# Kernel tuning notes

Hardware: AMD Instinct MI355X
Metric: run time of the kernel (lower is better)

The kernel has to match this reference:

```python
import jax, jax.numpy as jnp
import numpy as np

N = 100000
C_IN = 256          # in_channels == out_channels * expansion -> identity downsample
C_MID = 64          # out_channels
C_OUT = 256         # out_channels * expansion
K = 27              # 3x3x3 kernel offsets
EPS = 1e-6


def setup_inputs() -> dict:
    key = jax.random.key(0)
    ks = jax.random.split(key, 8)
    feats = jax.random.normal(ks[0], (N, C_IN), dtype=jnp.float32)
    neighbor_idx = jax.random.randint(ks[1], (N, K), 0, N, dtype=jnp.int32)
    # conv weights (torchsparse Conv3d: no bias)
    W1 = jax.random.normal(ks[2], (C_IN, C_MID), dtype=jnp.float32) * (1.0 / np.sqrt(C_IN))
    W2 = jax.random.normal(ks[3], (K, C_MID, C_MID), dtype=jnp.float32) * (1.0 / np.sqrt(K * C_MID))
    W3 = jax.random.normal(ks[4], (C_MID, C_OUT), dtype=jnp.float32) * (1.0 / np.sqrt(C_MID))
    # LayerNorm params
    g1 = jnp.ones((C_MID,), jnp.float32); b1 = jnp.zeros((C_MID,), jnp.float32)
    g2 = jnp.ones((C_MID,), jnp.float32); b2 = jnp.zeros((C_MID,), jnp.float32)
    g3 = jnp.ones((C_OUT,), jnp.float32); b3 = jnp.zeros((C_OUT,), jnp.float32)
    return {"feats": feats, "neighbor_idx": neighbor_idx,
            "W1": W1, "g1": g1, "b1": b1,
            "W2": W2, "g2": g2, "b2": b2,
            "W3": W3, "g3": g3, "b3": b3}


def _layernorm(x, g, b):
    # per-point LayerNorm over channel dim, eps=1e-6
    mu = jnp.mean(x, axis=-1, keepdims=True)
    var = jnp.mean(jnp.square(x - mu), axis=-1, keepdims=True)
    return (x - mu) * jax.lax.rsqrt(var + EPS) * g + b


def reference(feats, neighbor_idx, W1, g1, b1, W2, g2, b2, W3, g3, b3):
    # conv1 (1x1x1): per-point matmul -> LN -> ReLU
    h = jax.nn.relu(_layernorm(feats @ W1, g1, b1))               # [N, C_MID]
    # conv2 (3x3x3 sparse): gather neighbors, contract over (k, c)
    gathered = h[neighbor_idx]                                     # [N, K, C_MID]
    h2 = jnp.einsum('nkc,kcd->nd', gathered, W2)                   # [N, C_MID]
    h2 = jax.nn.relu(_layernorm(h2, g2, b2))
    # conv3 (1x1x1) -> LN
    h3 = _layernorm(h2 @ W3, g3, b3)                               # [N, C_OUT]
    # identity downsample (in_channels == out_channels*expansion, stride=1)
    return jax.nn.relu(h3 + feats)
```

## Files before the change

kernel.cpp:

```cpp
#include <hip/hip_runtime.h>

#define NPTS 100000
typedef unsigned short u16;
typedef __attribute__((ext_vector_type(8))) short short8;
typedef __attribute__((ext_vector_type(4))) float floatx4;

#define HOFF     (1u << 20)
#define H2OFF    (HOFF + 25600000u)
#define WS_NEED  (H2OFF + 25600000u)

__device__ __forceinline__ float bf2f(u16 u) {
    union { unsigned i; float f; } v; v.i = ((unsigned)u) << 16; return v.f;
}
__device__ __forceinline__ u16 f2bf(float f) {
    union { float fv; unsigned i; } v; v.fv = f;
    unsigned x = v.i;
    return (u16)((x + 0x7FFFu + ((x >> 16) & 1u)) >> 16);
}
__device__ __forceinline__ bool probe_bf16(const void* g1) {
    return ((const u16*)g1)[0] == 0x3F80u;
}
template<bool BF> __device__ __forceinline__ float ldf(const void* p, size_t i) {
    if constexpr (BF) return bf2f(((const u16*)p)[i]);
    else return ((const float*)p)[i];
}

template<bool BF> __device__ __forceinline__ void stout(char* ob, int r, int c, float v) {
    if constexpr (BF) ((u16*)(ob + (size_t)r * 512))[c] = f2bf(v);
    else ((float*)(ob + (size_t)r * 1024))[c] = v;
}

template<bool BF> __device__ __forceinline__ void prep_impl(
    const void* W2, const void* W1, const void* W3,
    u16* W2H, u16* W2L, u16* W1TH, u16* W1TL, u16* W3TH, u16* W3TL, int i)
{
    if (i < 27 * 4096) {
        int k = i >> 12, r = i & 4095, d = r >> 6, c = r & 63;
        float w = ldf<BF>(W2, (size_t)k * 4096 + c * 64 + d);
        u16 h = f2bf(w);
        W2H[i] = h;
        W2L[i] = f2bf(w - bf2f(h));
    } else if (i < 27 * 4096 + 16384) {
        int j = i - 27 * 4096;
        int d = j >> 8, k = j & 255;
        float w = ldf<BF>(W1, (size_t)k * 64 + d);
        u16 h = f2bf(w);
        W1TH[j] = h;
        W1TL[j] = f2bf(w - bf2f(h));
    } else if (i < 27 * 4096 + 32768) {
        int j = i - 27 * 4096 - 16384;
        int c = j >> 6, d = j & 63;
        float w = ldf<BF>(W3, (size_t)d * 256 + c);
        u16 h = f2bf(w);
        W3TH[j] = h;
        W3TL[j] = f2bf(w - bf2f(h));
    }
}
__global__ __launch_bounds__(256) void prep_k(const void* W2, const void* W1, const void* W3,
                                              const void* g1,
                                              u16* W2H, u16* W2L, u16* W1TH, u16* W1TL,
                                              u16* W3TH, u16* W3TL) {
    int i = blockIdx.x * 256 + threadIdx.x;
    if (probe_bf16(g1)) prep_impl<true >(W2, W1, W3, W2H, W2L, W1TH, W1TL, W3TH, W3TL, i);
    else                prep_impl<false>(W2, W1, W3, W2H, W2L, W1TH, W1TL, W3TH, W3TL, i);
}

template<bool BF> __device__ __forceinline__ void k1_impl(
    const void* feats, const u16* __restrict__ W1TH, const u16* __restrict__ W1TL,
    const void* g1, const void* b1, char* ob, u16* hb, int dense, u16* BH)
{
    u16* hbase = dense ? hb : (u16*)(ob + (BF ? 256 : 512));
    const int hpitch = dense ? 128 : (BF ? 256 : 512);

    const int tid = threadIdx.x;
    const int blk0 = blockIdx.x * 64;

    for (int j = tid; j < 2048; j += 256) {
        int d = j >> 5, c0 = (j & 31) * 8;
        *(int4*)&BH[d * 264 + c0] = ((const int4*)W1TH)[j];
    }
    __syncthreads();

    const int wave = tid >> 6, lane = tid & 63;
    const int q = lane >> 4, l15 = lane & 15;
    int pr = blk0 + wave * 16 + l15;
    if (pr >= NPTS) pr = NPTS - 1;

    floatx4 acc[4] = {};
    #pragma unroll
    for (int ks = 0; ks < 8; ++ks) {
        const int k0 = ks * 32;
        short8 ahi, alo;
        if constexpr (BF) {
            ahi = *(const short8*)((const u16*)feats + (size_t)pr * 256 + k0 + q * 8);
        } else {
            const float* fp = (const float*)feats + (size_t)pr * 256 + k0 + q * 8;
            float4 f0 = *(const float4*)fp;
            float4 f1 = *(const float4*)(fp + 4);
            float fv[8] = {f0.x, f0.y, f0.z, f0.w, f1.x, f1.y, f1.z, f1.w};
            #pragma unroll
            for (int j = 0; j < 8; ++j) {
                u16 h = f2bf(fv[j]);
                ahi[j] = (short)h;
                alo[j] = (short)f2bf(fv[j] - bf2f(h));
            }
        }
        #pragma unroll
        for (int t = 0; t < 4; ++t) {
            short8 bhi = *(const short8*)&BH[(t * 16 + l15) * 264 + k0 + q * 8];
            acc[t] = __builtin_amdgcn_mfma_f32_16x16x32_bf16(ahi, bhi, acc[t], 0, 0, 0);
            if constexpr (!BF) {
                short8 blo = *(const short8*)(W1TL + (size_t)(t * 16 + l15) * 256 + k0 + q * 8);
                acc[t] = __builtin_amdgcn_mfma_f32_16x16x32_bf16(alo, bhi, acc[t], 0, 0, 0);
                acc[t] = __builtin_amdgcn_mfma_f32_16x16x32_bf16(ahi, blo, acc[t], 0, 0, 0);
                acc[t] = __builtin_amdgcn_mfma_f32_16x16x32_bf16(alo, blo, acc[t], 0, 0, 0);
            }
        }
    }

    float gch[4], bch[4];
    #pragma unroll
    for (int t = 0; t < 4; ++t) { gch[t] = ldf<BF>(g1, t * 16 + l15); bch[t] = ldf<BF>(b1, t * 16 + l15); }

    const int p0 = blk0 + wave * 16;
    #pragma unroll
    for (int r = 0; r < 4; ++r) {
        float x0 = acc[0][r], x1 = acc[1][r], x2 = acc[2][r], x3 = acc[3][r];
        float s1 = x0 + x1 + x2 + x3;
        #pragma unroll
        for (int o = 1; o < 16; o <<= 1) s1 += __shfl_xor(s1, o);
        float mu = s1 * (1.f / 64.f);
        float c0 = x0 - mu, c1 = x1 - mu, c2 = x2 - mu, c3 = x3 - mu;
        float s2 = c0 * c0 + c1 * c1 + c2 * c2 + c3 * c3;
        #pragma unroll
        for (int o = 1; o < 16; o <<= 1) s2 += __shfl_xor(s2, o);
        float rs = rsqrtf(s2 * (1.f / 64.f) + 1e-6f);
        int prow = p0 + q * 4 + r;
        if (prow < NPTS) {
            u16* hp = hbase + (size_t)prow * hpitch;
            float cc[4] = {c0, c1, c2, c3};
            #pragma unroll
            for (int t = 0; t < 4; ++t) {
                float v = cc[t] * rs * gch[t] + bch[t];
                v = v > 0.f ? v : 0.f;
                int d = t * 16 + l15;
                u16 hi = f2bf(v);
                hp[d]      = hi;
                hp[64 + d] = f2bf(v - bf2f(hi));
            }
        }
    }
}
__global__ __launch_bounds__(256) void k1_k(const void* feats, const u16* W1TH, const u16* W1TL,
                                            const void* g1, const void* b1, char* ob,
                                            u16* hb, int dense)
{
    __shared__ __align__(16) u16 BH[64 * 264];
    if (probe_bf16(g1)) k1_impl<true >(feats, W1TH, W1TL, g1, b1, ob, hb, dense, BH);
    else                k1_impl<false>(feats, W1TH, W1TL, g1, b1, ob, hb, dense, BH);
}

__device__ __forceinline__ void k2_epilogue(
    floatx4* acc, const float* gch, const float* bch,
    float* h2base, int h2pitch, int p0, int q, int l15)
{
    #pragma unroll
    for (int r = 0; r < 4; ++r) {
        float x0 = acc[0][r], x1 = acc[1][r], x2 = acc[2][r], x3 = acc[3][r];
        float s1 = x0 + x1 + x2 + x3;
        #pragma unroll
        for (int o = 1; o < 16; o <<= 1) s1 += __shfl_xor(s1, o);
        float mu = s1 * (1.f / 64.f);
        float c0 = x0 - mu, c1 = x1 - mu, c2 = x2 - mu, c3 = x3 - mu;
        float s2 = c0 * c0 + c1 * c1 + c2 * c2 + c3 * c3;
        #pragma unroll
        for (int o = 1; o < 16; o <<= 1) s2 += __shfl_xor(s2, o);
        float rs = rsqrtf(s2 * (1.f / 64.f) + 1e-6f);
        int prow = p0 + q * 4 + r;
        if (prow < NPTS) {
            float* pp = h2base + (size_t)prow * h2pitch;
            float cc[4] = {c0, c1, c2, c3};
            #pragma unroll
            for (int t = 0; t < 4; ++t) {
                float v = cc[t] * rs * gch[t] + bch[t];
                pp[t * 16 + l15] = v > 0.f ? v : 0.f;
            }
        }
    }
}

__global__ __launch_bounds__(256) void k2bf_k(const int* __restrict__ nidx, const u16* __restrict__ W2H,
                                              const void* g2, const void* b2,
                                              const void* g1, char* ob, u16* hb, float* h2b, int dense)
{
    if (!probe_bf16(g1)) return;
    __shared__ __align__(16) u16 Bs[2 * 64 * 72];
    __shared__ int lidx[64 * 27];

    const u16* hbase = dense ? hb : (const u16*)(ob + 256);
    const int hpitch = dense ? 128 : 256;
    float* h2base = dense ? h2b : (float*)ob;
    const int h2pitch = dense ? 64 : 128;

    const int tid = threadIdx.x;
    const int blk0 = blockIdx.x * 64;

    for (int j = tid; j < 64 * 27; j += 256) {
        int p = blk0 + j / 27;
        if (p >= NPTS) p = NPTS - 1;
        lidx[j] = nidx[(size_t)p * 27 + (j % 27)];
    }

    const int wave = tid >> 6, lane = tid & 63;
    const int q = lane >> 4, l15 = lane & 15;
    const int ml = wave * 16 + l15;

    const int sd0 = (tid >> 3) * 72 + (tid & 7) * 8;
    const int sd1 = sd0 + 32 * 72;

    {
        int4 a0 = ((const int4*)W2H)[tid];
        int4 a1 = ((const int4*)W2H)[tid + 256];
        *(int4*)&Bs[sd0] = a0;
        *(int4*)&Bs[sd1] = a1;
    }
    __syncthreads();

    const u16* hp0 = hbase + (size_t)lidx[ml * 27] * hpitch;
    short8 ah0 = *(const short8*)(hp0 + q * 8);
    short8 ah1 = *(const short8*)(hp0 + 32 + q * 8);
    short8 al0 = *(const short8*)(hp0 + 64 + q * 8);
    short8 al1 = *(const short8*)(hp0 + 96 + q * 8);

    floatx4 acc[4] = {};
    int cur = 0;
    #pragma unroll 2
    for (int k = 0; k < 27; ++k) {
        const bool more = (k < 26);
        int4 nh0, nh1;
        if (more) {
            const int4* sH = (const int4*)(W2H + (size_t)(k + 1) * 4096);
            nh0 = sH[tid];
            nh1 = sH[tid + 256];
        }
        short8 ca0 = ah0, ca1 = ah1, cl0 = al0, cl1 = al1;
        if (more) {
            const u16* hn = hbase + (size_t)lidx[ml * 27 + k + 1] * hpitch;
            ah0 = *(const short8*)(hn + q * 8);
            ah1 = *(const short8*)(hn + 32 + q * 8);
            al0 = *(const short8*)(hn + 64 + q * 8);
            al1 = *(const short8*)(hn + 96 + q * 8);
        }
        __builtin_amdgcn_sched_barrier(0);
        const u16* BH = Bs + cur * 4608;
        #pragma unroll
        for (int t = 0; t < 4; ++t) {
            short8 b0 = *(const short8*)&BH[(t * 16 + l15) * 72 + q * 8];
            short8 b1 = *(const short8*)&BH[(t * 16 + l15) * 72 + 32 + q * 8];
            acc[t] = __builtin_amdgcn_mfma_f32_16x16x32_bf16(ca0, b0, acc[t], 0, 0, 0);
            acc[t] = __builtin_amdgcn_mfma_f32_16x16x32_bf16(ca1, b1, acc[t], 0, 0, 0);
            acc[t] = __builtin_amdgcn_mfma_f32_16x16x32_bf16(cl0, b0, acc[t], 0, 0, 0);
            acc[t] = __builtin_amdgcn_mfma_f32_16x16x32_bf16(cl1, b1, acc[t], 0, 0, 0);
        }
        if (more) {
            u16* dH = Bs + (cur ^ 1) * 4608;
            *(int4*)&dH[sd0] = nh0;
            *(int4*)&dH[sd1] = nh1;
        }
        __syncthreads();
        cur ^= 1;
    }

    float gch[4], bch[4];
    #pragma unroll
    for (int t = 0; t < 4; ++t) { gch[t] = ldf<true>(g2, t * 16 + l15); bch[t] = ldf<true>(b2, t * 16 + l15); }
    k2_epilogue(acc, gch, bch, h2base, h2pitch, blk0 + wave * 16, q, l15);
}

__global__ __launch_bounds__(256) void k2f32_k(const int* __restrict__ nidx,
                                               const u16* __restrict__ W2H, const u16* __restrict__ W2L,
                                               const void* g2, const void* b2,
                                               const void* g1, char* ob, u16* hb, float* h2b, int dense)
{
    if (probe_bf16(g1)) return;
    __shared__ __align__(16) u16 Bs[2 * 64 * 72];
    __shared__ int lidx[64 * 27];
    u16* BsH = Bs;
    u16* BsL = Bs + 4608;

    const u16* hbase = dense ? hb : (const u16*)(ob + 512);
    const int hpitch = dense ? 128 : 512;
    float* h2base = dense ? h2b : (float*)(ob + 768);
    const int h2pitch = dense ? 64 : 256;

    const int tid = threadIdx.x;
    const int blk0 = blockIdx.x * 64;

    for (int j = tid; j < 64 * 27; j += 256) {
        int p = blk0 + j / 27;
        if (p >= NPTS) p = NPTS - 1;
        lidx[j] = nidx[(size_t)p * 27 + (j % 27)];
    }
    __syncthreads();

    const int wave = tid >> 6, lane = tid & 63;
    const int q = lane >> 4, l15 = lane & 15;
    const int ml = wave * 16 + l15;

    const u16* hp0 = hbase + (size_t)lidx[ml * 27] * hpitch;
    short8 ah0 = *(const short8*)(hp0 + q * 8);
    short8 ah1 = *(const short8*)(hp0 + 32 + q * 8);
    short8 al0 = *(const short8*)(hp0 + 64 + q * 8);
    short8 al1 = *(const short8*)(hp0 + 96 + q * 8);

    floatx4 acc[4] = {};
    for (int k = 0; k < 27; ++k) {
        __syncthreads();
        for (int j = tid; j < 512; j += 256) {
            int d = j >> 3, c0 = (j & 7) * 8;
            *(int4*)&BsH[d * 72 + c0] = ((const int4*)(W2H + (size_t)k * 4096))[j];
        }
        for (int j = tid; j < 512; j += 256) {
            int d = j >> 3, c0 = (j & 7) * 8;
            *(int4*)&BsL[d * 72 + c0] = ((const int4*)(W2L + (size_t)k * 4096))[j];
        }
        __syncthreads();

        short8 ca0 = ah0, ca1 = ah1, cl0 = al0, cl1 = al1;
        if (k < 26) {
            const u16* hn = hbase + (size_t)lidx[ml * 27 + k + 1] * hpitch;
            ah0 = *(const short8*)(hn + q * 8);
            ah1 = *(const short8*)(hn + 32 + q * 8);
            al0 = *(const short8*)(hn + 64 + q * 8);
            al1 = *(const short8*)(hn + 96 + q * 8);
        }
        #pragma unroll
        for (int t = 0; t < 4; ++t) {
            short8 b0 = *(const short8*)&BsH[(t * 16 + l15) * 72 + q * 8];
            short8 b1 = *(const short8*)&BsH[(t * 16 + l15) * 72 + 32 + q * 8];
            acc[t] = __builtin_amdgcn_mfma_f32_16x16x32_bf16(ca0, b0, acc[t], 0, 0, 0);
            acc[t] = __builtin_amdgcn_mfma_f32_16x16x32_bf16(ca1, b1, acc[t], 0, 0, 0);
            acc[t] = __builtin_amdgcn_mfma_f32_16x16x32_bf16(cl0, b0, acc[t], 0, 0, 0);
            acc[t] = __builtin_amdgcn_mfma_f32_16x16x32_bf16(cl1, b1, acc[t], 0, 0, 0);
            short8 bl0 = *(const short8*)&BsL[(t * 16 + l15) * 72 + q * 8];
            short8 bl1 = *(const short8*)&BsL[(t * 16 + l15) * 72 + 32 + q * 8];
            acc[t] = __builtin_amdgcn_mfma_f32_16x16x32_bf16(ca0, bl0, acc[t], 0, 0, 0);
            acc[t] = __builtin_amdgcn_mfma_f32_16x16x32_bf16(ca1, bl1, acc[t], 0, 0, 0);
        }
    }

    float gch[4], bch[4];
    #pragma unroll
    for (int t = 0; t < 4; ++t) { gch[t] = ldf<false>(g2, t * 16 + l15); bch[t] = ldf<false>(b2, t * 16 + l15); }
    k2_epilogue(acc, gch, bch, h2base, h2pitch, blk0 + wave * 16, q, l15);
}

template<bool BF> __device__ __forceinline__ void k3_impl(
    const void* feats, const u16* __restrict__ W3TH, const u16* __restrict__ W3TL,
    const void* g3, const void* b3, char* ob, float* h2b, int dense, u16* BH)
{
    const float* h2base = dense ? h2b : (const float*)(ob + (BF ? 0 : 768));
    const int h2pitch = dense ? 64 : (BF ? 128 : 256);

    const int tid = threadIdx.x;
    const int blk0 = blockIdx.x * 64;

    for (int j = tid; j < 2048; j += 256) {
        int d = j >> 3, c0 = (j & 7) * 8;
        *(int4*)&BH[d * 72 + c0] = ((const int4*)W3TH)[j];
    }
    __syncthreads();

    const int wave = tid >> 6, lane = tid & 63;
    const int q = lane >> 4, l15 = lane & 15;
    int pr = blk0 + wave * 16 + l15;
    if (pr >= NPTS) pr = NPTS - 1;
    const float* h2p = h2base + (size_t)pr * h2pitch;

    floatx4 acc[16] = {};
    #pragma unroll
    for (int ks = 0; ks < 2; ++ks) {
        const int k0 = ks * 32;
        short8 ahi, alo;
        {
            const float* fp = h2p + k0 + q * 8;
            float4 f0 = *(const float4*)fp;
            float4 f1 = *(const float4*)(fp + 4);
            float fv[8] = {f0.x, f0.y, f0.z, f0.w, f1.x, f1.y, f1.z, f1.w};
            #pragma unroll
            for (int j = 0; j < 8; ++j) {
                u16 h = f2bf(fv[j]);
                ahi[j] = (short)h;
                alo[j] = (short)f2bf(fv[j] - bf2f(h));
            }
        }
        #pragma unroll
        for (int t = 0; t < 16; ++t) {
            short8 bhi = *(const short8*)&BH[(t * 16 + l15) * 72 + k0 + q * 8];
            acc[t] = __builtin_amdgcn_mfma_f32_16x16x32_bf16(ahi, bhi, acc[t], 0, 0, 0);
            acc[t] = __builtin_amdgcn_mfma_f32_16x16x32_bf16(alo, bhi, acc[t], 0, 0, 0);
            if constexpr (!BF) {
                short8 blo = *(const short8*)(W3TL + (size_t)(t * 16 + l15) * 64 + k0 + q * 8);
                acc[t] = __builtin_amdgcn_mfma_f32_16x16x32_bf16(ahi, blo, acc[t], 0, 0, 0);
                acc[t] = __builtin_amdgcn_mfma_f32_16x16x32_bf16(alo, blo, acc[t], 0, 0, 0);
            }
        }
    }

    float gch[16], bch[16];
    #pragma unroll
    for (int t = 0; t < 16; ++t) { gch[t] = ldf<BF>(g3, t * 16 + l15); bch[t] = ldf<BF>(b3, t * 16 + l15); }

    const int p0 = blk0 + wave * 16;
    #pragma unroll
    for (int r = 0; r < 4; ++r) {
        int prow = p0 + q * 4 + r;
        float s1 = 0.f;
        #pragma unroll
        for (int t = 0; t < 16; ++t) s1 += acc[t][r];
        #pragma unroll
        for (int o = 1; o < 16; o <<= 1) s1 += __shfl_xor(s1, o);
        float mu = s1 * (1.f / 256.f);
        float xc[16], s2 = 0.f;
        #pragma unroll
        for (int t = 0; t < 16; ++t) { xc[t] = acc[t][r] - mu; s2 += xc[t] * xc[t]; }
        #pragma unroll
        for (int o = 1; o < 16; o <<= 1) s2 += __shfl_xor(s2, o);
        float rs = rsqrtf(s2 * (1.f / 256.f) + 1e-6f);
        if (prow < NPTS) {
            #pragma unroll
            for (int t = 0; t < 16; ++t) {
                int c = t * 16 + l15;
                float v = xc[t] * rs * gch[t] + bch[t] + ldf<BF>(feats, (size_t)prow * 256 + c);
                stout<BF>(ob, prow, c, v > 0.f ? v : 0.f);
            }
        }
    }
}
__global__ __launch_bounds__(256) void k3_k(const void* feats, const u16* W3TH, const u16* W3TL,
                                            const void* g3, const void* b3,
                                            const void* g1, char* ob, float* h2b, int dense)
{
    __shared__ __align__(16) u16 BH[256 * 72];
    if (probe_bf16(g1)) k3_impl<true >(feats, W3TH, W3TL, g3, b3, ob, h2b, dense, BH);
    else                k3_impl<false>(feats, W3TH, W3TL, g3, b3, ob, h2b, dense, BH);
}

extern "C" void kernel_launch(void* const* d_in, const int* in_sizes, int n_in,
                              void* d_out, int out_size, void* d_ws, size_t ws_size,
                              hipStream_t stream) {
    const void* feats = d_in[0];
    const int*  nidx  = (const int*)d_in[1];
    const void* W1 = d_in[2];
    const void* g1 = d_in[3];
    const void* b1 = d_in[4];
    const void* W2 = d_in[5];
    const void* g2 = d_in[6];
    const void* b2 = d_in[7];
    const void* W3 = d_in[8];
    const void* g3 = d_in[9];
    const void* b3 = d_in[10];
    char* ob = (char*)d_out;

    char* ws = (char*)d_ws;
    u16* W2H  = (u16*)ws;
    u16* W2L  = (u16*)(ws + 221184);
    u16* W1TH = (u16*)(ws + 442368);
    u16* W1TL = (u16*)(ws + 475136);
    u16* W3TH = (u16*)(ws + 507904);
    u16* W3TL = (u16*)(ws + 540672);

    const int dense = (ws_size >= (size_t)WS_NEED) ? 1 : 0;
    u16*   hb  = (u16*)(ws + HOFF);
    float* h2b = (float*)(ws + H2OFF);

    prep_k<<<(27 * 4096 + 32768 + 255) / 256, 256, 0, stream>>>(W2, W1, W3, g1,
                                                                W2H, W2L, W1TH, W1TL, W3TH, W3TL);

    const int nblk = (NPTS + 63) / 64;
    k1_k<<<nblk, 256, 0, stream>>>(feats, W1TH, W1TL, g1, b1, ob, hb, dense);
    k2bf_k<<<nblk, 256, 0, stream>>>(nidx, W2H, g2, b2, g1, ob, hb, h2b, dense);
    k2f32_k<<<nblk, 256, 0, stream>>>(nidx, W2H, W2L, g2, b2, g1, ob, hb, h2b, dense);
    k3_k<<<nblk, 256, 0, stream>>>(feats, W3TH, W3TL, g3, b3, g1, ob, h2b, dense);
}
```

Before: 480.8 us.

## Double-buffer W2 high-half in LDS and read low-half weights from global

The fp32-path sparse conv kernel now prefetches the next kernel offset's high-part weights into registers and writes them into an alternate LDS buffer after the MFMAs. This removes one barrier per iteration and overlaps the weight fetch with compute. The low-part weights are read directly from global/L2 per lane instead of being staged in LDS. This trades LDS traffic and a sync for extra global-load latency inside the MFMA loop.

```diff
diff --git a/kernel.cpp b/kernel.cpp
--- a/kernel.cpp
+++ b/kernel.cpp
@@ -285,8 +285,6 @@
     if (probe_bf16(g1)) return;
     __shared__ __align__(16) u16 Bs[2 * 64 * 72];
     __shared__ int lidx[64 * 27];
-    u16* BsH = Bs;
-    u16* BsL = Bs + 4608;
 
     const u16* hbase = dense ? hb : (const u16*)(ob + 512);
     const int hpitch = dense ? 128 : 512;
@@ -301,11 +299,21 @@
         if (p >= NPTS) p = NPTS - 1;
         lidx[j] = nidx[(size_t)p * 27 + (j % 27)];
     }
-    __syncthreads();
 
     const int wave = tid >> 6, lane = tid & 63;
     const int q = lane >> 4, l15 = lane & 15;
     const int ml = wave * 16 + l15;
+
+    const int sd0 = (tid >> 3) * 72 + (tid & 7) * 8;
+    const int sd1 = sd0 + 32 * 72;
+
+    {
+        int4 a0 = ((const int4*)W2H)[tid];
+        int4 a1 = ((const int4*)W2H)[tid + 256];
+        *(int4*)&Bs[sd0] = a0;
+        *(int4*)&Bs[sd1] = a1;
+    }
+    __syncthreads();
 
     const u16* hp0 = hbase + (size_t)lidx[ml * 27] * hpitch;
     short8 ah0 = *(const short8*)(hp0 + q * 8);
@@ -314,39 +322,47 @@
     short8 al1 = *(const short8*)(hp0 + 96 + q * 8);
 
     floatx4 acc[4] = {};
+    int cur = 0;
+    #pragma unroll 2
     for (int k = 0; k < 27; ++k) {
-        __syncthreads();
-        for (int j = tid; j < 512; j += 256) {
-            int d = j >> 3, c0 = (j & 7) * 8;
-            *(int4*)&BsH[d * 72 + c0] = ((const int4*)(W2H + (size_t)k * 4096))[j];
-        }
-        for (int j = tid; j < 512; j += 256) {
-            int d = j >> 3, c0 = (j & 7) * 8;
-            *(int4*)&BsL[d * 72 + c0] = ((const int4*)(W2L + (size_t)k * 4096))[j];
-        }
-        __syncthreads();
-
+        const bool more = (k < 26);
+        int4 nh0, nh1;
+        if (more) {
+            const int4* sH = (const int4*)(W2H + (size_t)(k + 1) * 4096);
+            nh0 = sH[tid];
+            nh1 = sH[tid + 256];
+        }
         short8 ca0 = ah0, ca1 = ah1, cl0 = al0, cl1 = al1;
-        if (k < 26) {
+        if (more) {
             const u16* hn = hbase + (size_t)lidx[ml * 27 + k + 1] * hpitch;
             ah0 = *(const short8*)(hn + q * 8);
             ah1 = *(const short8*)(hn + 32 + q * 8);
             al0 = *(const short8*)(hn + 64 + q * 8);
             al1 = *(const short8*)(hn + 96 + q * 8);
         }
+        __builtin_amdgcn_sched_barrier(0);
+        const u16* BH = Bs + cur * 4608;
+        const u16* WL = W2L + (size_t)k * 4096;
         #pragma unroll
         for (int t = 0; t < 4; ++t) {
-            short8 b0 = *(const short8*)&BsH[(t * 16 + l15) * 72 + q * 8];
-            short8 b1 = *(const short8*)&BsH[(t * 16 + l15) * 72 + 32 + q * 8];
+            short8 b0 = *(const short8*)&BH[(t * 16 + l15) * 72 + q * 8];
+            short8 b1 = *(const short8*)&BH[(t * 16 + l15) * 72 + 32 + q * 8];
             acc[t] = __builtin_amdgcn_mfma_f32_16x16x32_bf16(ca0, b0, acc[t], 0, 0, 0);
             acc[t] = __builtin_amdgcn_mfma_f32_16x16x32_bf16(ca1, b1, acc[t], 0, 0, 0);
             acc[t] = __builtin_amdgcn_mfma_f32_16x16x32_bf16(cl0, b0, acc[t], 0, 0, 0);
             acc[t] = __builtin_amdgcn_mfma_f32_16x16x32_bf16(cl1, b1, acc[t], 0, 0, 0);
-            short8 bl0 = *(const short8*)&BsL[(t * 16 + l15) * 72 + q * 8];
-            short8 bl1 = *(const short8*)&BsL[(t * 16 + l15) * 72 + 32 + q * 8];
+            short8 bl0 = *(const short8*)(WL + (t * 16 + l15) * 64 + q * 8);
+            short8 bl1 = *(const short8*)(WL + (t * 16 + l15) * 64 + 32 + q * 8);
             acc[t] = __builtin_amdgcn_mfma_f32_16x16x32_bf16(ca0, bl0, acc[t], 0, 0, 0);
             acc[t] = __builtin_amdgcn_mfma_f32_16x16x32_bf16(ca1, bl1, acc[t], 0, 0, 0);
         }
+        if (more) {
+            u16* dH = Bs + (cur ^ 1) * 4608;
+            *(int4*)&dH[sd0] = nh0;
+            *(int4*)&dH[sd1] = nh1;
+        }
+        __syncthreads();
+        cur ^= 1;
     }
 
     float gch[4], bch[4];
```

After: 601.3 us. 25.1% more time.
